# Optimization experiments

Measured on AMD Instinct MI355X. Metric: run time of the kernel, lower is better.

Reference implementation:

```python
import jax, jax.numpy as jnp
import numpy as np

B, H, W, C = 16, 64, 64, 256
WS = 8          # window_size
SHIFT = 4       # shift_size
HEADS = 8
HEAD_DIM = C // HEADS
N = WS * WS     # tokens per window
HID = 4 * C     # mlp hidden
EPS = 1e-5


def _rel_pos_index():
    coords = np.stack(np.meshgrid(np.arange(WS), np.arange(WS), indexing='ij'))  # [2,WS,WS]
    flat = coords.reshape(2, -1)                                                  # [2,N]
    rel = (flat[:, :, None] - flat[:, None, :]).transpose(1, 2, 0)                # [N,N,2]
    rel[:, :, 0] += WS - 1
    rel[:, :, 1] += WS - 1
    rel[:, :, 0] *= 2 * WS - 1
    return rel.sum(-1).astype(np.int32)                                           # [N,N]


def _attn_mask():
    # shifted-window region ids, identical to get_img_mask (shift == WS//2)
    img = np.zeros((H, W), dtype=np.float32)
    cnt = 0
    for hs in (slice(0, H - WS), slice(H - WS, H - SHIFT), slice(H - SHIFT, H)):
        for ws_ in (slice(0, W - WS), slice(W - WS, W - SHIFT), slice(W - SHIFT, W)):
            img[hs, ws_] = cnt
            cnt += 1
    mw = img.reshape(H // WS, WS, W // WS, WS).transpose(0, 2, 1, 3).reshape(-1, N)  # [nW,N]
    diff = mw[:, None, :] - mw[:, :, None]
    return np.where(diff != 0, -100.0, 0.0).astype(np.float32)                        # [nW,N,N]


def window_partition(x):
    # [B,H,W,C] -> [B*nW, N, C]
    x = x.reshape(B, H // WS, WS, W // WS, WS, C)
    return x.transpose(0, 1, 3, 2, 4, 5).reshape(-1, N, C)


def window_reverse(w):
    # [B*nW, WS, WS, C] -> [B,H,W,C]
    x = w.reshape(B, H // WS, W // WS, WS, WS, C)
    return x.transpose(0, 1, 3, 2, 4, 5).reshape(B, H, W, C)


def layernorm(x, g, b):
    mu = jnp.mean(x, -1, keepdims=True)
    var = jnp.mean(jnp.square(x - mu), -1, keepdims=True)
    return (x - mu) * jax.lax.rsqrt(var + EPS) * g + b


def setup_inputs() -> dict:
    key = jax.random.key(0)
    ks = jax.random.split(key, 12)
    s = 0.02
    return {
        'x': jax.random.normal(ks[0], (B, H, W, C), jnp.float32),
        'ln1_g': jnp.ones((C,), jnp.float32),
        'ln1_b': jnp.zeros((C,), jnp.float32),
        'qkv_w': jax.random.normal(ks[1], (C, 3 * C), jnp.float32) * s,
        'qkv_b': jnp.zeros((3 * C,), jnp.float32),
        'proj_w': jax.random.normal(ks[2], (C, C), jnp.float32) * s,
        'proj_b': jnp.zeros((C,), jnp.float32),
        'rel_bias_table': jax.random.normal(ks[3], ((2 * WS - 1) ** 2, HEADS), jnp.float32) * s,
        'ln2_g': jnp.ones((C,), jnp.float32),
        'ln2_b': jnp.zeros((C,), jnp.float32),
        'mlp_w1': jax.random.normal(ks[4], (C, HID), jnp.float32) * s,
        'mlp_b1': jnp.zeros((HID,), jnp.float32),
        'mlp_w2': jax.random.normal(ks[5], (HID, C), jnp.float32) * s,
        'mlp_b2': jnp.zeros((C,), jnp.float32),
        'rel_index': jnp.asarray(_rel_pos_index()),  # [N,N] int32, constant
    }


def reference(x, ln1_g, ln1_b, qkv_w, qkv_b, proj_w, proj_b, rel_bias_table,
              ln2_g, ln2_b, mlp_w1, mlp_b1, mlp_w2, mlp_b2, rel_index):
    attn_mask = jnp.asarray(_attn_mask())                 # [nW,N,N]
    nW = attn_mask.shape[0]

    shortcut = x.reshape(B, H * W, C)
    h = layernorm(shortcut, ln1_g, ln1_b).reshape(B, H, W, C)

    # cyclic shift + window partition
    h = jnp.roll(h, shift=(-SHIFT, -SHIFT), axis=(1, 2))
    xw = window_partition(h)                              # [B*nW, N, C]

    # window attention with relative position bias
    qkv = xw @ qkv_w + qkv_b                              # [B*nW, N, 3C]
    qkv = qkv.reshape(-1, N, 3, HEADS, HEAD_DIM).transpose(2, 0, 3, 1, 4)
    q, k, v = qkv[0], qkv[1], qkv[2]                      # [B*nW, heads, N, hd]
    attn = jnp.einsum('whnd,whmd->whnm', q * (HEAD_DIM ** -0.5), k)
    bias = rel_bias_table[rel_index]                      # [N,N,heads]
    attn = attn + bias.transpose(2, 0, 1)[None]           # [B*nW,heads,N,N]
    attn = attn.reshape(B, nW, HEADS, N, N) + attn_mask[None, :, None]
    attn = jax.nn.softmax(attn.reshape(-1, HEADS, N, N), axis=-1)
    out = jnp.einsum('whnm,whmd->whnd', attn, v)
    out = out.transpose(0, 2, 1, 3).reshape(-1, N, C)
    out = out @ proj_w + proj_b                           # [B*nW, N, C]

    # window reverse + reverse shift
    out = window_reverse(out.reshape(-1, WS, WS, C))
    out = jnp.roll(out, shift=(SHIFT, SHIFT), axis=(1, 2)).reshape(B, H * W, C)

    h = shortcut + out
    m = layernorm(h, ln2_g, ln2_b)
    m = jax.nn.gelu(m @ mlp_w1 + mlp_b1) @ mlp_w2 + mlp_b2
    h = h + m
    return h.reshape(B, H, W, C)
```

## Files before the change

### kernel.cpp

```cpp
#include <hip/hip_runtime.h>


typedef __attribute__((ext_vector_type(8))) short bf16x8;
typedef __attribute__((ext_vector_type(4))) float f32x4;
typedef __attribute__((ext_vector_type(16))) float f32x16;

__device__ __forceinline__ float bf2f(unsigned short h) {
    union { unsigned int u; float f; } c; c.u = ((unsigned int)h) << 16; return c.f;
}
__device__ __forceinline__ unsigned short f2bf(float f) {
    union { float f; unsigned int u; } c; c.f = f;
    unsigned int u = c.u;
    return (unsigned short)((u + 0x7FFFu + ((u >> 16) & 1u)) >> 16);
}
__device__ __forceinline__ unsigned int cvtpk_bf16(float lo, float hi) {
    unsigned int r;
    asm volatile("v_cvt_pk_bf16_f32 %0, %1, %2" : "=v"(r) : "v"(lo), "v"(hi));
    return r;
}
__device__ __forceinline__ void perm32swap(unsigned int& a, unsigned int& b) {
    asm volatile("v_permlane32_swap_b32 %0, %1" : "+v"(a), "+v"(b));
}
__device__ __forceinline__ int remap_row(int row) {
    int b  = row >> 12;
    int w6 = (row >> 6) & 63;
    int n  = row & 63;
    int hp = (((w6 >> 3) << 3) + (n >> 3) + 4) & 63;
    int wp = (((w6 & 7) << 3) + (n & 7) + 4) & 63;
    return (b << 12) | (hp << 6) | wp;
}
__device__ __forceinline__ float gelu_f(float v) {
    float u = 1.5957691216057308f * (v + 0.044715f * v * v * v);
    return v / (1.0f + __expf(-u));
}
__device__ __forceinline__ void gload16(const unsigned short* g, unsigned short* l) {
    __builtin_amdgcn_global_load_lds(
        (const __attribute__((address_space(1))) void*)g,
        (__attribute__((address_space(3))) void*)l, 16, 0, 0);
}

__global__ __launch_bounds__(256) void ln_kernel(
    const float* __restrict__ in, const float* __restrict__ g,
    const float* __restrict__ b, unsigned short* __restrict__ out, int remap)
{
    int wave = threadIdx.x >> 6, lane = threadIdx.x & 63;
    int row = (blockIdx.x << 2) + wave;
    int src = remap ? remap_row(row) : row;
    float4 xv = *(const float4*)(in + (size_t)src * 256 + (lane << 2));
    float s  = xv.x + xv.y + xv.z + xv.w;
    float ss = xv.x*xv.x + xv.y*xv.y + xv.z*xv.z + xv.w*xv.w;
#pragma unroll
    for (int off = 32; off; off >>= 1) {
        s  += __shfl_xor(s,  off, 64);
        ss += __shfl_xor(ss, off, 64);
    }
    float mu  = s * (1.0f / 256.0f);
    float inv = rsqrtf(ss * (1.0f / 256.0f) - mu * mu + 1e-5f);
    float4 gv = *(const float4*)(g + (lane << 2));
    float4 bv = *(const float4*)(b + (lane << 2));
    ushort4 o;
    o.x = f2bf((xv.x - mu) * inv * gv.x + bv.x);
    o.y = f2bf((xv.y - mu) * inv * gv.y + bv.y);
    o.z = f2bf((xv.z - mu) * inv * gv.z + bv.z);
    o.w = f2bf((xv.w - mu) * inv * gv.w + bv.w);
    *(ushort4*)(out + (size_t)row * 256 + (lane << 2)) = o;
}

__device__ __forceinline__ void convT_body(
    const float* __restrict__ in, unsigned short* __restrict__ out,
    int K, int N, int b, float (*t)[33], int tid)
{
    int kb = K >> 5;
    int bk = (b % kb) << 5;
    int bn = (b / kb) << 5;
    int r = tid >> 5, c = tid & 31;
#pragma unroll
    for (int i = 0; i < 4; ++i)
        t[r + i * 8][c] = in[(size_t)(bk + r + i * 8) * N + bn + c];
    __syncthreads();
#pragma unroll
    for (int i = 0; i < 4; ++i)
        out[(size_t)(bn + r + i * 8) * K + bk + c] = f2bf(t[c][r + i * 8]);
}

__global__ __launch_bounds__(256) void prep_kernel(
    const float* __restrict__ qkv_w, const float* __restrict__ proj_w,
    const float* __restrict__ w1, const float* __restrict__ w2,
    unsigned short* __restrict__ qkvT, unsigned short* __restrict__ prjT,
    unsigned short* __restrict__ w1T, unsigned short* __restrict__ w2T,
    const float* __restrict__ table, const int* __restrict__ relidx,
    float* __restrict__ bexp)
{
    __shared__ float t[32][33];
    const int b = blockIdx.x, tid = threadIdx.x;
    if      (b < 192) convT_body(qkv_w, qkvT, 256,  768, b,       t, tid);
    else if (b < 256) convT_body(proj_w, prjT, 256,  256, b - 192, t, tid);
    else if (b < 512) convT_body(w1,    w1T,  256, 1024, b - 256, t, tid);
    else if (b < 768) convT_body(w2,    w2T, 1024,  256, b - 512, t, tid);
    else {
        int i = (b - 768) * 256 + tid;
        int head = i >> 12;
        int q = (i >> 6) & 63;
        int k = i & 63;
        bexp[i] = table[relidx[q * 64 + k] * 8 + head];
    }
}

template<int OUT_BF16, int DO_GELU, int RESID, int QSCALE>
__global__ __launch_bounds__(512, 4) void mgemm_kernel(
    const unsigned short* __restrict__ A, const unsigned short* __restrict__ BT,
    const float* __restrict__ bias, void* __restrict__ outp,
    const float* __restrict__ resid, int M, int N, int K)
{
    __shared__ unsigned short As[2][128 * 32];
    __shared__ unsigned short Bs[2][128 * 32];

    const int cpx = (int)gridDim.x >> 3;
    const int bid = ((int)blockIdx.x & 7) * cpx + ((int)blockIdx.x >> 3);

    const int nb = N >> 7;
    const int m0 = (bid / nb) << 7;
    const int n0 = (bid % nb) << 7;
    const int tid  = threadIdx.x;
    const int wid  = tid >> 6;
    const int lane = tid & 63;
    const int wm = (wid >> 1) << 5;
    const int wn = (wid & 1) << 6;

    const unsigned short* Ag = A  + (size_t)m0 * K;
    const unsigned short* Bg = BT + (size_t)n0 * K;
    const size_t ra = (size_t)(tid >> 2) * K + (((tid & 3) ^ ((tid >> 2) & 3)) << 3);

    f32x4 acc[4][2] = {};
    const int fr = lane & 15;
    const int fq = lane >> 4;
    const int axor = ((fq ^ (fr & 3)) << 3);

#define STAGE(buf, kk)                                                        \
    {                                                                         \
        gload16(Ag + ra + (kk), As[buf] + tid * 8);                           \
        gload16(Bg + ra + (kk), Bs[buf] + tid * 8);                           \
    }

    STAGE(0, 0);
    STAGE(1, 32);
    asm volatile("s_waitcnt vmcnt(2)" ::: "memory");
    __builtin_amdgcn_s_barrier();
    __builtin_amdgcn_sched_barrier(0);

    for (int k0 = 0; k0 < K; k0 += 32) {
        const int cur = (k0 >> 5) & 1;
        bf16x8 af[2], bfr[4];
#pragma unroll
        for (int i = 0; i < 2; ++i)
            af[i] = *(const bf16x8*)(As[cur] + (wm + i * 16 + fr) * 32 + axor);
#pragma unroll
        for (int j = 0; j < 4; ++j)
            bfr[j] = *(const bf16x8*)(Bs[cur] + (wn + j * 16 + fr) * 32 + axor);
#pragma unroll
        for (int j = 0; j < 4; ++j)
#pragma unroll
            for (int i = 0; i < 2; ++i)
                acc[j][i] = __builtin_amdgcn_mfma_f32_16x16x32_bf16(
                    bfr[j], af[i], acc[j][i], 0, 0, 0);

        if (k0 + 32 < K) {
            __builtin_amdgcn_s_barrier();
            if (k0 + 64 < K) {
                STAGE(cur, k0 + 64);
                asm volatile("s_waitcnt vmcnt(2)" ::: "memory");
            } else {
                asm volatile("s_waitcnt vmcnt(0)" ::: "memory");
            }
            __builtin_amdgcn_s_barrier();
            __builtin_amdgcn_sched_barrier(0);
        }
    }
#undef STAGE

#pragma unroll
    for (int j = 0; j < 4; ++j) {
        const int colbase = n0 + wn + j * 16 + (fq << 2);
        const float4 b4 = *(const float4*)(bias + colbase);
#pragma unroll
        for (int i = 0; i < 2; ++i) {
            const int row = m0 + wm + i * 16 + fr;
            float v0 = acc[j][i][0] + b4.x;
            float v1 = acc[j][i][1] + b4.y;
            float v2 = acc[j][i][2] + b4.z;
            float v3 = acc[j][i][3] + b4.w;
            if (QSCALE && colbase < 256) {
                v0 *= 0.17677669529663687f; v1 *= 0.17677669529663687f;
                v2 *= 0.17677669529663687f; v3 *= 0.17677669529663687f;
            }
            if (DO_GELU) {
                v0 = gelu_f(v0); v1 = gelu_f(v1); v2 = gelu_f(v2); v3 = gelu_f(v3);
            }
            if (OUT_BF16) {
                uint2 pp;
                pp.x = cvtpk_bf16(v0, v1);
                pp.y = cvtpk_bf16(v2, v3);
                *(uint2*)((unsigned short*)outp + (size_t)row * N + colbase) = pp;
            } else {
                const int orow = (RESID == 2) ? remap_row(row) : row;
                float4 o4;
                if (RESID) {
                    const float4 r4 = *(const float4*)(resid + (size_t)orow * N + colbase);
                    o4.x = v0 + r4.x; o4.y = v1 + r4.y;
                    o4.z = v2 + r4.z; o4.w = v3 + r4.w;
                } else {
                    o4.x = v0; o4.y = v1; o4.z = v2; o4.w = v3;
                }
                *(float4*)((float*)outp + (size_t)orow * N + colbase) = o4;
            }
        }
    }
}

__global__ __launch_bounds__(64, 3) void attn_kernel(
    const unsigned short* __restrict__ qkv,
    const float* __restrict__ bexp,
    unsigned short* __restrict__ out)
{
    __shared__ unsigned short VT[2048];
    const int bid  = blockIdx.x;
    const int widx = bid & 1023;
    const int head = bid >> 10;
    const int l  = threadIdx.x;
    const int lo = l & 31, hi = l >> 5;

    const unsigned short* base = qkv + (size_t)widx * 64 * 768;

#pragma unroll
    for (int c = 0; c < 4; ++c) {
        union { bf16x8 v; unsigned short s[8]; } u;
        u.v = *(const bf16x8*)(base + (size_t)l * 768 + 512 + head * 32 + c * 8);
#pragma unroll
        for (int e = 0; e < 8; ++e) {
            int d = c * 8 + e;
            int wb = ((d * 64 + l) * 2) ^ ((d & 7) << 4);
            *(unsigned short*)((char*)VT + wb) = u.s[e];
        }
    }

    f32x16 acc[2][2] = {};
#pragma unroll
    for (int kd = 0; kd < 2; ++kd) {
        const int coff = head * 32 + kd * 16 + hi * 8;
        bf16x8 kf0 = *(const bf16x8*)(base + (size_t)lo        * 768 + 256 + coff);
        bf16x8 kf1 = *(const bf16x8*)(base + (size_t)(32 + lo) * 768 + 256 + coff);
        bf16x8 qf0 = *(const bf16x8*)(base + (size_t)lo        * 768 + coff);
        bf16x8 qf1 = *(const bf16x8*)(base + (size_t)(32 + lo) * 768 + coff);
        acc[0][0] = __builtin_amdgcn_mfma_f32_32x32x16_bf16(kf0, qf0, acc[0][0], 0, 0, 0);
        acc[0][1] = __builtin_amdgcn_mfma_f32_32x32x16_bf16(kf0, qf1, acc[0][1], 0, 0, 0);
        acc[1][0] = __builtin_amdgcn_mfma_f32_32x32x16_bf16(kf1, qf0, acc[1][0], 0, 0, 0);
        acc[1][1] = __builtin_amdgcn_mfma_f32_32x32x16_bf16(kf1, qf1, acc[1][1], 0, 0, 0);
    }

#pragma unroll
    for (int qb = 0; qb < 2; ++qb) {
        const float* bq = bexp + head * 4096 + (qb * 32 + lo) * 64;
#pragma unroll
        for (int kb = 0; kb < 2; ++kb)
#pragma unroll
            for (int j = 0; j < 4; ++j) {
                float4 b4 = *(const float4*)(bq + kb * 32 + j * 8 + hi * 4);
                acc[kb][qb][4 * j + 0] += b4.x;
                acc[kb][qb][4 * j + 1] += b4.y;
                acc[kb][qb][4 * j + 2] += b4.z;
                acc[kb][qb][4 * j + 3] += b4.w;
            }
    }

    const int w6 = widx & 63;
    if (((w6 >> 3) == 7) || ((w6 & 7) == 7)) {
#pragma unroll
        for (int qb = 0; qb < 2; ++qb) {
            int nq = qb * 32 + lo;
            int phq = ((w6 >> 3) << 3) + (nq >> 3), pwq = ((w6 & 7) << 3) + (nq & 7);
            int rq = ((phq < 56) ? 0 : ((phq < 60) ? 1 : 2)) * 3
                   + ((pwq < 56) ? 0 : ((pwq < 60) ? 1 : 2));
#pragma unroll
            for (int kb = 0; kb < 2; ++kb)
#pragma unroll
                for (int r = 0; r < 16; ++r) {
                    int nk = kb * 32 + (r & 3) + 8 * (r >> 2) + 4 * hi;
                    int phk = ((w6 >> 3) << 3) + (nk >> 3), pwk = ((w6 & 7) << 3) + (nk & 7);
                    int rk = ((phk < 56) ? 0 : ((phk < 60) ? 1 : 2)) * 3
                           + ((pwk < 56) ? 0 : ((pwk < 60) ? 1 : 2));
                    if (rk != rq) acc[kb][qb][r] -= 100.0f;
                }
        }
    }

#pragma unroll
    for (int qb = 0; qb < 2; ++qb) {
        float mx = acc[0][qb][0];
#pragma unroll
        for (int r = 1; r < 16; ++r) mx = fmaxf(mx, acc[0][qb][r]);
#pragma unroll
        for (int r = 0; r < 16; ++r) mx = fmaxf(mx, acc[1][qb][r]);
        mx = fmaxf(mx, __shfl_xor(mx, 32, 64));
        float sum = 0.f;
#pragma unroll
        for (int kb = 0; kb < 2; ++kb)
#pragma unroll
            for (int r = 0; r < 16; ++r) {
                float e = __expf(acc[kb][qb][r] - mx);
                acc[kb][qb][r] = e;
                sum += e;
            }
        sum += __shfl_xor(sum, 32, 64);
        float inv = 1.0f / sum;
#pragma unroll
        for (int kb = 0; kb < 2; ++kb)
#pragma unroll
            for (int r = 0; r < 16; ++r) acc[kb][qb][r] *= inv;
    }

    f32x16 o[2] = {};
#pragma unroll
    for (int ks = 0; ks < 4; ++ks) {
        const int s8 = (ks & 1) * 8, kb = ks >> 1;
        const int rb = ((lo * 64 + 16 * ks + 8 * hi) * 2) ^ ((lo & 7) << 4);
        bf16x8 vb = *(const bf16x8*)((const char*)VT + rb);
#pragma unroll
        for (int qb = 0; qb < 2; ++qb) {
            unsigned int a0 = cvtpk_bf16(acc[kb][qb][s8 + 0], acc[kb][qb][s8 + 1]);
            unsigned int b0 = cvtpk_bf16(acc[kb][qb][s8 + 4], acc[kb][qb][s8 + 5]);
            unsigned int a1 = cvtpk_bf16(acc[kb][qb][s8 + 2], acc[kb][qb][s8 + 3]);
            unsigned int b1 = cvtpk_bf16(acc[kb][qb][s8 + 6], acc[kb][qb][s8 + 7]);
            perm32swap(a0, b0);
            perm32swap(a1, b1);
            union { unsigned int u[4]; bf16x8 v; } w;
            w.u[0] = a0; w.u[1] = a1; w.u[2] = b0; w.u[3] = b1;
            o[qb] = __builtin_amdgcn_mfma_f32_32x32x16_bf16(w.v, vb, o[qb], 0, 0, 0);
        }
    }

    unsigned short* ob = out + (size_t)widx * 64 * 256 + head * 32 + lo;
#pragma unroll
    for (int qb = 0; qb < 2; ++qb)
#pragma unroll
        for (int r = 0; r < 16; ++r) {
            int q = qb * 32 + (r & 3) + 8 * (r >> 2) + 4 * hi;
            ob[(size_t)q * 256] = f2bf(o[qb][r]);
        }
}

extern "C" void kernel_launch(void* const* d_in, const int* in_sizes, int n_in,
                              void* d_out, int out_size, void* d_ws, size_t ws_size,
                              hipStream_t stream)
{
    const float* x      = (const float*)d_in[0];
    const float* ln1_g  = (const float*)d_in[1];
    const float* ln1_b  = (const float*)d_in[2];
    const float* qkv_w  = (const float*)d_in[3];
    const float* qkv_b  = (const float*)d_in[4];
    const float* proj_w = (const float*)d_in[5];
    const float* proj_b = (const float*)d_in[6];
    const float* table  = (const float*)d_in[7];
    const float* ln2_g  = (const float*)d_in[8];
    const float* ln2_b  = (const float*)d_in[9];
    const float* w1     = (const float*)d_in[10];
    const float* b1     = (const float*)d_in[11];
    const float* w2     = (const float*)d_in[12];
    const float* b2     = (const float*)d_in[13];
    const int*   relidx = (const int*)d_in[14];
    float* out = (float*)d_out;

    char* w = (char*)d_ws;
    unsigned short* xw   = (unsigned short*)w;
    unsigned short* qkvb = (unsigned short*)(w + (32u << 20));
    float*          h2   = (float*)(w + (160u << 20));
    float*          bexp = (float*)(w + (224u << 20));
    unsigned short* qkvT = (unsigned short*)(w + (224u << 20) + (128u << 10));
    unsigned short* prjT = qkvT + 768 * 256;
    unsigned short* w1T  = prjT + 256 * 256;
    unsigned short* w2T  = w1T + 1024 * 256;

    prep_kernel<<<896, 256, 0, stream>>>(qkv_w, proj_w, w1, w2,
                                         qkvT, prjT, w1T, w2T,
                                         table, relidx, bexp);
    ln_kernel<<<16384, 256, 0, stream>>>(x, ln1_g, ln1_b, xw, 1);
    mgemm_kernel<1, 0, 0, 1><<<512 * 6, 512, 0, stream>>>(xw, qkvT, qkv_b, (void*)qkvb,
                                                          nullptr, 65536, 768, 256);
    attn_kernel<<<8192, 64, 0, stream>>>(qkvb, bexp, xw);
    mgemm_kernel<0, 0, 2, 0><<<512 * 2, 512, 0, stream>>>(xw, prjT, proj_b, (void*)h2,
                                                          x, 65536, 256, 256);
    ln_kernel<<<16384, 256, 0, stream>>>(h2, ln2_g, ln2_b, xw, 0);
    mgemm_kernel<1, 1, 0, 0><<<512 * 8, 512, 0, stream>>>(xw, w1T, b1, (void*)qkvb,
                                                          nullptr, 65536, 1024, 256);
    mgemm_kernel<0, 0, 1, 0><<<512 * 2, 512, 0, stream>>>(qkvb, w2T, b2, (void*)out,
                                                          h2, 65536, 256, 1024);
}
```

Measured before the change: 311.0 us.

## Add persistent K=256 GEMM keeping weight tile resident in LDS

```diff
diff --git a/kernel.cpp b/kernel.cpp
--- a/kernel.cpp
+++ b/kernel.cpp
@@ -107,6 +107,128 @@
 }
 
 template<int OUT_BF16, int DO_GELU, int RESID, int QSCALE>
+__global__ __launch_bounds__(512, 2) void pgemm_kernel(
+    const unsigned short* __restrict__ A, const unsigned short* __restrict__ BT,
+    const float* __restrict__ bias, void* __restrict__ outp,
+    const float* __restrict__ resid, int N, int G)
+{
+    __shared__ unsigned short Bl[128 * 256];
+    __shared__ unsigned short Al[2][64 * 256];
+
+    const int cpx = (int)gridDim.x >> 3;
+    const int bid = ((int)blockIdx.x & 7) * cpx + ((int)blockIdx.x >> 3);
+    const int ntile = bid / G;
+    const int g     = bid % G;
+    const int n0 = ntile << 7;
+
+    const int tid  = threadIdx.x;
+    const int lane = tid & 63;
+    const int wid  = tid >> 6;
+    const int wm = (wid >> 2) << 5;
+    const int wn = (wid & 3) << 5;
+    const int fr = lane & 15, fq = lane >> 4;
+
+    {
+        const unsigned short* Bg = BT + (size_t)n0 * 256;
+#pragma unroll
+        for (int i = 0; i < 8; ++i) {
+            int s = tid + (i << 9);
+            int r = s >> 5, p = s & 31;
+            int lg = (p & 24) | ((p ^ r) & 7);
+            gload16(Bg + (size_t)r * 256 + lg * 8, Bl + s * 8);
+        }
+    }
+#define STAGE_A(buf, mt)                                                      \
+    {                                                                         \
+        const unsigned short* Ag_ = A + (size_t)(mt) * 64 * 256;              \
+        _Pragma("unroll")                                                     \
+        for (int i_ = 0; i_ < 4; ++i_) {                                      \
+            int s_ = tid + (i_ << 9);                                         \
+            int r_ = s_ >> 5, p_ = s_ & 31;                                   \
+            int lg_ = (p_ & 24) | ((p_ ^ r_) & 7);                            \
+            gload16(Ag_ + (size_t)r_ * 256 + lg_ * 8, Al[buf] + s_ * 8);      \
+        }                                                                     \
+    }
+    STAGE_A(0, g);
+    asm volatile("s_waitcnt vmcnt(0)" ::: "memory");
+    __builtin_amdgcn_s_barrier();
+
+    int buf = 0;
+    for (int mt = g; mt < 1024; mt += G) {
+        if (mt + G < 1024) STAGE_A(buf ^ 1, mt + G);
+
+        f32x4 acc[2][2] = {};
+#pragma unroll
+        for (int it = 0; it < 8; ++it) {
+            bf16x8 af[2], bf[2];
+#pragma unroll
+            for (int i = 0; i < 2; ++i) {
+                int ar = wm + i * 16 + fr;
+                int kg = it * 4 + fq;
+                int p  = (kg & 24) | ((kg ^ ar) & 7);
+                af[i] = *(const bf16x8*)(Al[buf] + ar * 256 + p * 8);
+            }
+#pragma unroll
+            for (int j = 0; j < 2; ++j) {
+                int br = wn + j * 16 + fr;
+                int kg = it * 4 + fq;
+                int p  = (kg & 24) | ((kg ^ br) & 7);
+                bf[j] = *(const bf16x8*)(Bl + br * 256 + p * 8);
+            }
+#pragma unroll
+            for (int j = 0; j < 2; ++j)
+#pragma unroll
+                for (int i = 0; i < 2; ++i)
+                    acc[j][i] = __builtin_amdgcn_mfma_f32_16x16x32_bf16(
+                        bf[j], af[i], acc[j][i], 0, 0, 0);
+        }
+
+#pragma unroll
+        for (int j = 0; j < 2; ++j) {
+            const int colbase = n0 + wn + j * 16 + (fq << 2);
+            const float4 b4 = *(const float4*)(bias + colbase);
+#pragma unroll
+            for (int i = 0; i < 2; ++i) {
+                const int row = (mt << 6) + wm + i * 16 + fr;
+                float v0 = acc[j][i][0] + b4.x;
+                float v1 = acc[j][i][1] + b4.y;
+                float v2 = acc[j][i][2] + b4.z;
+                float v3 = acc[j][i][3] + b4.w;
+                if (QSCALE && colbase < 256) {
+                    v0 *= 0.17677669529663687f; v1 *= 0.17677669529663687f;
+                    v2 *= 0.17677669529663687f; v3 *= 0.17677669529663687f;
+                }
+                if (DO_GELU) {
+                    v0 = gelu_f(v0); v1 = gelu_f(v1); v2 = gelu_f(v2); v3 = gelu_f(v3);
+                }
+                if (OUT_BF16) {
+                    uint2 pp;
+                    pp.x = cvtpk_bf16(v0, v1);
+                    pp.y = cvtpk_bf16(v2, v3);
+                    *(uint2*)((unsigned short*)outp + (size_t)row * N + colbase) = pp;
+                } else {
+                    const int orow = (RESID == 2) ? remap_row(row) : row;
+                    float4 o4;
+                    if (RESID) {
+                        const float4 r4 = *(const float4*)(resid + (size_t)orow * N + colbase);
+                        o4.x = v0 + r4.x; o4.y = v1 + r4.y;
+                        o4.z = v2 + r4.z; o4.w = v3 + r4.w;
+                    } else {
+                        o4.x = v0; o4.y = v1; o4.z = v2; o4.w = v3;
+                    }
+                    *(float4*)((float*)outp + (size_t)orow * N + colbase) = o4;
+                }
+            }
+        }
+
+        asm volatile("s_waitcnt vmcnt(0)" ::: "memory");
+        __builtin_amdgcn_s_barrier();
+        buf ^= 1;
+    }
+#undef STAGE_A
+}
+
+template<int OUT_BF16, int DO_GELU, int RESID, int QSCALE>
 __global__ __launch_bounds__(512, 4) void mgemm_kernel(
     const unsigned short* __restrict__ A, const unsigned short* __restrict__ BT,
     const float* __restrict__ bias, void* __restrict__ outp,
@@ -141,7 +263,6 @@
         gload16(Ag + ra + (kk), As[buf] + tid * 8);                           \
         gload16(Bg + ra + (kk), Bs[buf] + tid * 8);                           \
     }
-
     STAGE(0, 0);
     STAGE(1, 32);
     asm volatile("s_waitcnt vmcnt(2)" ::: "memory");
@@ -383,14 +504,14 @@
                                          qkvT, prjT, w1T, w2T,
                                          table, relidx, bexp);
     ln_kernel<<<16384, 256, 0, stream>>>(x, ln1_g, ln1_b, xw, 1);
-    mgemm_kernel<1, 0, 0, 1><<<512 * 6, 512, 0, stream>>>(xw, qkvT, qkv_b, (void*)qkvb,
-                                                          nullptr, 65536, 768, 256);
+    pgemm_kernel<1, 0, 0, 1><<<6 * 64, 512, 0, stream>>>(xw, qkvT, qkv_b, (void*)qkvb,
+                                                         nullptr, 768, 64);
     attn_kernel<<<8192, 64, 0, stream>>>(qkvb, bexp, xw);
-    mgemm_kernel<0, 0, 2, 0><<<512 * 2, 512, 0, stream>>>(xw, prjT, proj_b, (void*)h2,
-                                                          x, 65536, 256, 256);
+    pgemm_kernel<0, 0, 2, 0><<<2 * 128, 512, 0, stream>>>(xw, prjT, proj_b, (void*)h2,
+                                                          x, 256, 128);
     ln_kernel<<<16384, 256, 0, stream>>>(h2, ln2_g, ln2_b, xw, 0);
-    mgemm_kernel<1, 1, 0, 0><<<512 * 8, 512, 0, stream>>>(xw, w1T, b1, (void*)qkvb,
-                                                          nullptr, 65536, 1024, 256);
+    pgemm_kernel<1, 1, 0, 0><<<8 * 48, 512, 0, stream>>>(xw, w1T, b1, (void*)qkvb,
+                                                         nullptr, 1024, 48);
     mgemm_kernel<0, 0, 1, 0><<<512 * 2, 512, 0, stream>>>(qkvb, w2T, b2, (void*)out,
                                                           h2, 65536, 256, 1024);
 }
```

After: 383.9 us. 23.4% more time.

## Deepen GEMM pipeline to four LDS stages and store residual stream in bf16

Applied to the files above, without the earlier changes.

```diff
diff --git a/kernel.cpp b/kernel.cpp
--- a/kernel.cpp
+++ b/kernel.cpp
@@ -39,14 +39,21 @@
         (__attribute__((address_space(3))) void*)l, 16, 0, 0);
 }
 
+template<int INBF>
 __global__ __launch_bounds__(256) void ln_kernel(
-    const float* __restrict__ in, const float* __restrict__ g,
+    const void* __restrict__ inp, const float* __restrict__ g,
     const float* __restrict__ b, unsigned short* __restrict__ out, int remap)
 {
     int wave = threadIdx.x >> 6, lane = threadIdx.x & 63;
     int row = (blockIdx.x << 2) + wave;
     int src = remap ? remap_row(row) : row;
-    float4 xv = *(const float4*)(in + (size_t)src * 256 + (lane << 2));
+    float4 xv;
+    if (INBF) {
+        ushort4 u = *(const ushort4*)((const unsigned short*)inp + (size_t)src * 256 + (lane << 2));
+        xv.x = bf2f(u.x); xv.y = bf2f(u.y); xv.z = bf2f(u.z); xv.w = bf2f(u.w);
+    } else {
+        xv = *(const float4*)((const float*)inp + (size_t)src * 256 + (lane << 2));
+    }
     float s  = xv.x + xv.y + xv.z + xv.w;
     float ss = xv.x*xv.x + xv.y*xv.y + xv.z*xv.z + xv.w*xv.w;
 #pragma unroll
@@ -106,14 +113,14 @@
     }
 }
 
-template<int OUT_BF16, int DO_GELU, int RESID, int QSCALE>
-__global__ __launch_bounds__(512, 4) void mgemm_kernel(
+template<int OUT_BF16, int DO_GELU, int RESID, int QSCALE, int RESBF>
+__global__ __launch_bounds__(512, 2) void mgemm_kernel(
     const unsigned short* __restrict__ A, const unsigned short* __restrict__ BT,
     const float* __restrict__ bias, void* __restrict__ outp,
-    const float* __restrict__ resid, int M, int N, int K)
-{
-    __shared__ unsigned short As[2][128 * 32];
-    __shared__ unsigned short Bs[2][128 * 32];
+    const void* __restrict__ resid, int M, int N, int K)
+{
+    __shared__ unsigned short As[4][128 * 32];
+    __shared__ unsigned short Bs[4][128 * 32];
 
     const int cpx = (int)gridDim.x >> 3;
     const int bid = ((int)blockIdx.x & 7) * cpx + ((int)blockIdx.x >> 3);
@@ -142,14 +149,18 @@
         gload16(Bg + ra + (kk), Bs[buf] + tid * 8);                           \
     }
 
+    const int NIT = K >> 5;
     STAGE(0, 0);
     STAGE(1, 32);
-    asm volatile("s_waitcnt vmcnt(2)" ::: "memory");
-    __builtin_amdgcn_s_barrier();
-    __builtin_amdgcn_sched_barrier(0);
-
-    for (int k0 = 0; k0 < K; k0 += 32) {
-        const int cur = (k0 >> 5) & 1;
+    STAGE(2, 64);
+
+    for (int t = 0; t < NIT; ++t) {
+        if (t + 2 < NIT)      asm volatile("s_waitcnt vmcnt(4)" ::: "memory");
+        else if (t + 1 < NIT) asm volatile("s_waitcnt vmcnt(2)" ::: "memory");
+        else                  asm volatile("s_waitcnt vmcnt(0)" ::: "memory");
+        __builtin_amdgcn_s_barrier();
+
+        const int cur = t & 3;
         bf16x8 af[2], bfr[4];
 #pragma unroll
         for (int i = 0; i < 2; ++i)
@@ -164,17 +175,7 @@
                 acc[j][i] = __builtin_amdgcn_mfma_f32_16x16x32_bf16(
                     bfr[j], af[i], acc[j][i], 0, 0, 0);
 
-        if (k0 + 32 < K) {
-            __builtin_amdgcn_s_barrier();
-            if (k0 + 64 < K) {
-                STAGE(cur, k0 + 64);
-                asm volatile("s_waitcnt vmcnt(2)" ::: "memory");
-            } else {
-                asm volatile("s_waitcnt vmcnt(0)" ::: "memory");
-            }
-            __builtin_amdgcn_s_barrier();
-            __builtin_amdgcn_sched_barrier(0);
-        }
+        if (t + 3 < NIT) STAGE((t + 3) & 3, (t + 3) << 5);
     }
 #undef STAGE
 
@@ -196,21 +197,27 @@
             if (DO_GELU) {
                 v0 = gelu_f(v0); v1 = gelu_f(v1); v2 = gelu_f(v2); v3 = gelu_f(v3);
             }
+            const int orow = (RESID == 2) ? remap_row(row) : row;
+            if (RESID) {
+                if (RESBF) {
+                    ushort4 r4 = *(const ushort4*)((const unsigned short*)resid
+                                                   + (size_t)orow * N + colbase);
+                    v0 += bf2f(r4.x); v1 += bf2f(r4.y);
+                    v2 += bf2f(r4.z); v3 += bf2f(r4.w);
+                } else {
+                    const float4 r4 = *(const float4*)((const float*)resid
+                                                       + (size_t)orow * N + colbase);
+                    v0 += r4.x; v1 += r4.y; v2 += r4.z; v3 += r4.w;
+                }
+            }
             if (OUT_BF16) {
                 uint2 pp;
                 pp.x = cvtpk_bf16(v0, v1);
                 pp.y = cvtpk_bf16(v2, v3);
-                *(uint2*)((unsigned short*)outp + (size_t)row * N + colbase) = pp;
+                *(uint2*)((unsigned short*)outp + (size_t)orow * N + colbase) = pp;
             } else {
-                const int orow = (RESID == 2) ? remap_row(row) : row;
                 float4 o4;
-                if (RESID) {
-                    const float4 r4 = *(const float4*)(resid + (size_t)orow * N + colbase);
-                    o4.x = v0 + r4.x; o4.y = v1 + r4.y;
-                    o4.z = v2 + r4.z; o4.w = v3 + r4.w;
-                } else {
-                    o4.x = v0; o4.y = v1; o4.z = v2; o4.w = v3;
-                }
+                o4.x = v0; o4.y = v1; o4.z = v2; o4.w = v3;
                 *(float4*)((float*)outp + (size_t)orow * N + colbase) = o4;
             }
         }
@@ -372,7 +379,7 @@
     char* w = (char*)d_ws;
     unsigned short* xw   = (unsigned short*)w;
     unsigned short* qkvb = (unsigned short*)(w + (32u << 20));
-    float*          h2   = (float*)(w + (160u << 20));
+    unsigned short* h2b  = (unsigned short*)(w + (160u << 20));
     float*          bexp = (float*)(w + (224u << 20));
     unsigned short* qkvT = (unsigned short*)(w + (224u << 20) + (128u << 10));
     unsigned short* prjT = qkvT + 768 * 256;
@@ -382,15 +389,15 @@
     prep_kernel<<<896, 256, 0, stream>>>(qkv_w, proj_w, w1, w2,
                                          qkvT, prjT, w1T, w2T,
                                          table, relidx, bexp);
-    ln_kernel<<<16384, 256, 0, stream>>>(x, ln1_g, ln1_b, xw, 1);
-    mgemm_kernel<1, 0, 0, 1><<<512 * 6, 512, 0, stream>>>(xw, qkvT, qkv_b, (void*)qkvb,
-                                                          nullptr, 65536, 768, 256);
+    ln_kernel<0><<<16384, 256, 0, stream>>>(x, ln1_g, ln1_b, xw, 1);
+    mgemm_kernel<1, 0, 0, 1, 0><<<512 * 6, 512, 0, stream>>>(
+        xw, qkvT, qkv_b, (void*)qkvb, nullptr, 65536, 768, 256);
     attn_kernel<<<8192, 64, 0, stream>>>(qkvb, bexp, xw);
-    mgemm_kernel<0, 0, 2, 0><<<512 * 2, 512, 0, stream>>>(xw, prjT, proj_b, (void*)h2,
-                                                          x, 65536, 256, 256);
-    ln_kernel<<<16384, 256, 0, stream>>>(h2, ln2_g, ln2_b, xw, 0);
-    mgemm_kernel<1, 1, 0, 0><<<512 * 8, 512, 0, stream>>>(xw, w1T, b1, (void*)qkvb,
-                                                          nullptr, 65536, 1024, 256);
-    mgemm_kernel<0, 0, 1, 0><<<512 * 2, 512, 0, stream>>>(qkvb, w2T, b2, (void*)out,
-                                                          h2, 65536, 256, 1024);
-}
+    mgemm_kernel<1, 0, 2, 0, 0><<<512 * 2, 512, 0, stream>>>(
+        xw, prjT, proj_b, (void*)h2b, x, 65536, 256, 256);
+    ln_kernel<1><<<16384, 256, 0, stream>>>(h2b, ln2_g, ln2_b, xw, 0);
+    mgemm_kernel<1, 1, 0, 0, 0><<<512 * 8, 512, 0, stream>>>(
+        xw, w1T, b1, (void*)qkvb, nullptr, 65536, 1024, 256);
+    mgemm_kernel<0, 0, 1, 0, 1><<<512 * 2, 512, 0, stream>>>(
+        qkvb, w2T, b2, (void*)out, h2b, 65536, 256, 1024);
+}
```

After: 314.5 us. Within noise of the previous version (+1.1%).
